# Performance work log

Measured on AMD Instinct MI355X. Metric: run time of the kernel, lower is better.

The kernel has to match this reference:

```python
import jax, jax.numpy as jnp
import numpy as np
from jax import lax

ALPHA = 1.5
N_ITER = 100


def entmax(z, alpha=ALPHA, n_iter=N_ITER):
    # z: [B, Sq, Sk] scores. Bisection for the entmax threshold tau.
    z = (alpha - 1.0) * z.astype(jnp.float32)
    S = z.shape[-1]
    z_max = jnp.max(z, axis=-1, keepdims=True)          # [B, Sq, 1]
    tau_min = z_max - 1.0
    tau_max = z_max - np.float32(S ** (1.0 - alpha))
    inv = 1.0 / (alpha - 1.0)                            # = 2.0 for alpha=1.5

    def body(carry, _):
        tmin, tmax, _ = carry
        tau = (tmin + tmax) * 0.5
        p = jnp.maximum(z - tau, 0.0) ** inv             # [B, Sq, Sk]
        Z = jnp.sum(p, axis=-1, keepdims=True)           # [B, Sq, 1]
        tmin = jnp.where(Z >= 1.0, tau, tmin)
        tmax = jnp.where(Z < 1.0, tau, tmax)
        return (tmin, tmax, tau), None

    init = (tau_min, tau_max, (tau_min + tau_max) * 0.5)
    (tmin, tmax, tau), _ = lax.scan(jax.checkpoint(body), init, None, length=n_iter)
    # faithful to the TF code: final output uses p, Z from the LAST iteration's tau
    p = jnp.maximum(z - tau, 0.0) ** inv
    Z = jnp.sum(p, axis=-1, keepdims=True)
    return p / Z


def setup_inputs() -> dict:
    key = jax.random.key(0)
    kq, kk, kv = jax.random.split(key, 3)
    B, S, D = 8, 2048, 128
    return {
        "query": jax.random.normal(kq, (B, S, D), dtype=jnp.float32),
        "key": jax.random.normal(kk, (B, S, D), dtype=jnp.float32),
        "value": jax.random.normal(kv, (B, S, D), dtype=jnp.float32),
    }


def reference(query, key, value):
    scores = jnp.einsum("bqd,bkd->bqk", query, key)      # QK^T, no scaling (as in source)
    weights = entmax(scores, alpha=ALPHA, n_iter=N_ITER)
    return jnp.einsum("bqk,bkd->bqd", weights, value)
```

## Files before the change

kernel.cpp:

```cpp
#include <hip/hip_runtime.h>

#define BB 8
#define SS 2048
#define DD 128
#define ROWS 16
#define NW 8
#define CTW 16

typedef short bf16x8 __attribute__((ext_vector_type(8)));
typedef float f32x4 __attribute__((ext_vector_type(4)));

template <int I> struct IC { static constexpr int value = I; };
template <int I, int N, typename F>
__device__ __forceinline__ void sfor(F&& f) {
  if constexpr (I < N) { f(IC<I>{}); sfor<I + 1, N>((F&&)f); }
}

__device__ __forceinline__ short f2bf(float x) {
  return __builtin_bit_cast(short, (__bf16)x);
}

__device__ __forceinline__ void stage_tile(const short* g, short* l) {
#pragma unroll
  for (int s = 0; s < 4; ++s) {
    __builtin_amdgcn_global_load_lds(
        (const __attribute__((address_space(1))) void*)(g + (s << 9)),
        (__attribute__((address_space(3))) void*)(l + (s << 9)), 16, 0, 0);
  }
}

__global__ __launch_bounds__(256)
void ksplit(const float* __restrict__ K, short* __restrict__ Khi) {
  const int lin = blockIdx.x * 256 + threadIdx.x;
  const int r   = lin >> 4;
  const int c8  = lin & 15;
  const float4 v0 = *(const float4*)(K + (size_t)lin * 8);
  const float4 v1 = *(const float4*)(K + (size_t)lin * 8 + 4);
  bf16x8 h;
  h[0] = f2bf(v0.x); h[1] = f2bf(v0.y); h[2] = f2bf(v0.z); h[3] = f2bf(v0.w);
  h[4] = f2bf(v1.x); h[5] = f2bf(v1.y); h[6] = f2bf(v1.z); h[7] = f2bf(v1.w);
  const int bct  = r >> 4;
  const int m16  = r & 15;
  const int s    = c8 >> 2;
  const int quad = c8 & 3;
  const size_t out = ((((size_t)bct * 4 + s) * 64) + quad * 16 + m16) * 8;
  *(bf16x8*)(Khi + out) = h;
}

__global__ __launch_bounds__(512) __attribute__((amdgpu_waves_per_eu(4)))
void attn(const float* __restrict__ Q, const short* __restrict__ Khi,
          const float* __restrict__ K, const float* __restrict__ V,
          float* __restrict__ Out) {
  __shared__ short kring[NW][2][2048];
  __shared__ unsigned short Qs[ROWS][136];
  __shared__ float rbuf[ROWS][64];
  __shared__ int   scol[ROWS][64];
  __shared__ float exM[NW][ROWS];
  __shared__ int   rcnt[ROWS];
  __shared__ int   rovf[ROWS];
  __shared__ float tauB[ROWS], ZB[ROWS];

  const int tid  = threadIdx.x;
  const int lane = tid & 63;
  const int wid  = __builtin_amdgcn_readfirstlane(tid >> 6);
  const int quad = lane >> 4, m16 = lane & 15;
  const int b    = blockIdx.x & 7;
  const int qt   = blockIdx.x >> 3;

  const float* Qb = Q + (size_t)(b * SS + qt * ROWS) * DD;
  const float* Kb = K + (size_t)b * SS * DD;
  const float* Vb = V + (size_t)b * SS * DD;
  float*       Ob = Out + (size_t)(b * SS + qt * ROWS) * DD;
  const short* KHb = Khi + (size_t)b * SS * DD;

  if (tid < ROWS) { rcnt[tid] = 0; rovf[tid] = 0; }

  {
    const int row = tid >> 5, d = (tid & 31) * 4;
    const float4 v = *(const float4*)&Qb[row * DD + d];
    ushort4 h;
    h.x = (unsigned short)f2bf(0.5f * v.x);
    h.y = (unsigned short)f2bf(0.5f * v.y);
    h.z = (unsigned short)f2bf(0.5f * v.z);
    h.w = (unsigned short)f2bf(0.5f * v.w);
    *(ushort4*)&Qs[row][d] = h;
  }
  __syncthreads();

  bf16x8 qh[4];
#pragma unroll
  for (int s = 0; s < 4; ++s)
    qh[s] = *(const bf16x8*)&Qs[m16][s * 32 + quad * 8];

  short* ring0 = &kring[wid][0][0];
  short* ring1 = &kring[wid][1][0];
  const short* gw = KHb + ((size_t)(wid * CTW) << 11) + lane * 8;

  stage_tile(gw + 0 * 2048, ring0);
  stage_tile(gw + 1 * 2048, ring1);

  f32x4 acc[CTW];
  sfor<0, CTW>([&](auto ic) {
    constexpr int i = ic.value;
    if constexpr (i < CTW - 1) asm volatile("s_waitcnt vmcnt(4)" ::: "memory");
    else                       asm volatile("s_waitcnt vmcnt(0)" ::: "memory");
    const short* sbl = ((i & 1) ? ring1 : ring0) + lane * 8;
    f32x4 c = {0.f, 0.f, 0.f, 0.f};
    sfor<0, 4>([&](auto sc) {
      constexpr int s = sc.value;
      const bf16x8 bh = *(const bf16x8*)(sbl + (s << 9));
      c = __builtin_amdgcn_mfma_f32_16x16x32_bf16(qh[s], bh, c, 0, 0, 0);
    });
    acc[i] = c;
    if constexpr (i + 2 < CTW) {
      asm volatile("s_waitcnt lgkmcnt(0)" ::: "memory");
      stage_tile(gw + (i + 2) * 2048, (i & 1) ? ring1 : ring0);
    }
  });

  float mx[4] = {-1e38f, -1e38f, -1e38f, -1e38f};
  sfor<0, CTW>([&](auto ic) {
#pragma unroll
    for (int j = 0; j < 4; ++j) mx[j] = fmaxf(mx[j], acc[ic.value][j]);
  });
#pragma unroll
  for (int j = 0; j < 4; ++j)
#pragma unroll
    for (int s = 1; s <= 8; s <<= 1) mx[j] = fmaxf(mx[j], __shfl_xor(mx[j], s));
  if (m16 == 0) {
#pragma unroll
    for (int j = 0; j < 4; ++j) exM[wid][4 * quad + j] = mx[j];
  }
  __syncthreads();
  float M4[4];
#pragma unroll
  for (int j = 0; j < 4; ++j) {
    float m = -1e38f;
#pragma unroll
    for (int w = 0; w < NW; ++w) m = fmaxf(m, exM[w][4 * quad + j]);
    M4[j] = m;
  }

  sfor<0, CTW>([&](auto ic) {
    constexpr int i = ic.value;
    const int col = wid * 256 + i * 16 + m16;
#pragma unroll
    for (int j = 0; j < 4; ++j) {
      const int row = 4 * quad + j;
      if (acc[i][j] > M4[j] - 1.25f) {
        const int pos = atomicAdd(&rcnt[row], 1);
        if (pos < 64) { scol[row][pos] = col; rbuf[row][pos] = acc[i][j]; }
        else rovf[row] = 1;
      }
    }
  });
  __syncthreads();

  const int rr32 = lane >> 5;
  const int row  = 2 * wid + rr32;
  const int l32  = lane & 31;
  const int nA = rcnt[2 * wid]     < 64 ? rcnt[2 * wid]     : 64;
  const int nB = rcnt[2 * wid + 1] < 64 ? rcnt[2 * wid + 1] : 64;
  const int nr  = rr32 ? nB : nA;
  const int nmx = nA > nB ? nA : nB;

  {
    const float4 q4 = *(const float4*)&Qb[row * DD + l32 * 4];
    for (int i = 0; i < nmx; ++i) {
      const bool act = i < nr;
      const int c = act ? scol[row][i] : scol[row][0];
      const float4 k4 = *(const float4*)&Kb[(size_t)c * DD + l32 * 4];
      float t = q4.x * k4.x + q4.y * k4.y + q4.z * k4.z + q4.w * k4.w;
#pragma unroll
      for (int s = 1; s <= 16; s <<= 1) t += __shfl_xor(t, s);
      if (act && l32 == 0) rbuf[row][i] = 0.5f * t;
    }
  }

  {
    const float z0 = (l32 < nr)      ? rbuf[row][l32]      : -1e38f;
    const float z1 = (l32 + 32 < nr) ? rbuf[row][l32 + 32] : -1e38f;
    float k0 = 0.f, S10 = 0.f, S20 = 0.f, nb0 = -1e38f;
    float k1 = 0.f, S11 = 0.f, S21 = 0.f, nb1 = -1e38f;
    for (int j = 0; j < nr; ++j) {
      const float w = rbuf[row][j];
      const bool ge0 = (w > z0) || (w == z0 && j <= l32);
      k0  += ge0 ? 1.f : 0.f;
      S10 += ge0 ? w : 0.f;
      S20  = ge0 ? fmaf(w, w, S20) : S20;
      nb0  = (!ge0 && w > nb0) ? w : nb0;
      const bool ge1 = (w > z1) || (w == z1 && j <= l32 + 32);
      k1  += ge1 ? 1.f : 0.f;
      S11 += ge1 ? w : 0.f;
      S21  = ge1 ? fmaf(w, w, S21) : S21;
      nb1  = (!ge1 && w > nb1) ? w : nb1;
    }
    const float d0 = fmaxf(fmaf(S10, S10, -k0 * (S20 - 1.f)), 0.f);
    const float d1 = fmaxf(fmaf(S11, S11, -k1 * (S21 - 1.f)), 0.f);
    const float tau0 = (S10 - __builtin_sqrtf(d0)) / fmaxf(k0, 1.f);
    const float tau1 = (S11 - __builtin_sqrtf(d1)) / fmaxf(k1, 1.f);
    const bool v0b = z0 > tau0, v1b = z1 > tau1;
    const bool v0  = v0b && (nb0 <= tau0);
    const bool v1  = v1b && (nb1 <= tau1);
    float tv = fmaxf(v0 ? tau0 : -1e38f, v1 ? tau1 : -1e38f);
    float tb = fmaxf(v0b ? tau0 : -1e38f, v1b ? tau1 : -1e38f);
#pragma unroll
    for (int s = 1; s <= 16; s <<= 1) {
      tv = fmaxf(tv, __shfl_xor(tv, s));
      tb = fmaxf(tb, __shfl_xor(tb, s));
    }
    const float tau = (tv > -1e37f) ? tv : tb;
    const float p0 = fmaxf(z0 - tau, 0.f);
    const float p1 = fmaxf(z1 - tau, 0.f);
    float zp = fmaf(p0, p0, p1 * p1);
#pragma unroll
    for (int s = 1; s <= 16; s <<= 1) zp += __shfl_xor(zp, s);
    if (l32 == 0) { tauB[row] = tau; ZB[row] = zp; }
  }

  if (!rovf[row]) {
    const float tau = tauB[row];
    const float iz  = 1.0f / ZB[row];
    float4 o = {0.f, 0.f, 0.f, 0.f};
    for (int i = 0; i < nr; ++i) {
      const float rv = rbuf[row][i];
      const float tt = fmaxf(rv - tau, 0.f);
      const float pi = tt * tt * iz;
      const int   c  = scol[row][i];
      const float4 v4 = *(const float4*)&Vb[(size_t)c * DD + l32 * 4];
      o.x = fmaf(pi, v4.x, o.x);
      o.y = fmaf(pi, v4.y, o.y);
      o.z = fmaf(pi, v4.z, o.z);
      o.w = fmaf(pi, v4.w, o.w);
    }
    *(float4*)&Ob[row * DD + l32 * 4] = o;
  }

#pragma unroll
  for (int rr = 0; rr < 2; ++rr) {
    const int frow = 2 * wid + rr;
    if (!rovf[frow]) continue;
    float* zr = (float*)&kring[wid][0][0];
    for (int c0 = 0; c0 < 32; ++c0) {
      const int c = c0 * 64 + lane;
      const float* kp = &Kb[(size_t)c * DD];
      float t = 0.f;
      for (int d = 0; d < DD; d += 4) {
        const float4 qv = *(const float4*)&Qb[frow * DD + d];
        const float4 kv = *(const float4*)&kp[d];
        t = fmaf(qv.x, kv.x, t); t = fmaf(qv.y, kv.y, t);
        t = fmaf(qv.z, kv.z, t); t = fmaf(qv.w, kv.w, t);
      }
      zr[c] = 0.5f * t;
    }
    float Mr = -1e38f;
    for (int c0 = 0; c0 < 32; ++c0) Mr = fmaxf(Mr, zr[c0 * 64 + lane]);
#pragma unroll
    for (int s = 1; s <= 32; s <<= 1) Mr = fmaxf(Mr, __shfl_xor(Mr, s));
    float tmn = Mr - 1.0f, tmx = Mr - 0.022097086912079608f;
    float tau = 0.5f * (tmn + tmx), Zr = 0.f;
    for (int it = 0; it < 100; ++it) {
      tau = 0.5f * (tmn + tmx);
      float zp = 0.f;
      for (int c0 = 0; c0 < 32; ++c0) {
        const float tt = fmaxf(zr[c0 * 64 + lane] - tau, 0.f);
        zp = fmaf(tt, tt, zp);
      }
#pragma unroll
      for (int s = 1; s <= 32; s <<= 1) zp += __shfl_xor(zp, s);
      Zr = zp;
      const float nmn = (zp >= 1.f) ? tau : tmn;
      const float nmx2 = (zp >= 1.f) ? tmx : tau;
      const bool ch = (nmn != tmn) || (nmx2 != tmx);
      tmn = nmn; tmx = nmx2;
      if (!__any(ch)) break;
    }
    const float iz = 1.0f / Zr;
    float2 o = {0.f, 0.f};
    for (int c = 0; c < SS; ++c) {
      const float tt = fmaxf(zr[c] - tau, 0.f);
      if (tt > 0.f) {
        const float pi = tt * tt * iz;
        const float2 v2 = *(const float2*)&Vb[(size_t)c * DD + lane * 2];
        o.x = fmaf(pi, v2.x, o.x);
        o.y = fmaf(pi, v2.y, o.y);
      }
    }
    *(float2*)&Ob[frow * DD + lane * 2] = o;
  }
}

extern "C" void kernel_launch(void* const* d_in, const int* in_sizes, int n_in,
                              void* d_out, int out_size, void* d_ws, size_t ws_size,
                              hipStream_t stream) {
  const float* Q = (const float*)d_in[0];
  const float* K = (const float*)d_in[1];
  const float* V = (const float*)d_in[2];
  float* out = (float*)d_out;
  short* Khi = (short*)d_ws;

  hipLaunchKernelGGL(ksplit, dim3(BB * SS * DD / (256 * 8)), dim3(256), 0, stream,
                     K, Khi);
  hipLaunchKernelGGL(attn, dim3(BB * (SS / ROWS)), dim3(512), 0, stream,
                     Q, Khi, K, V, out);
}
```

Measured before the change: 117.5 us.

## Halve warps per block and pack per-tile score accumulators as bf16 pairs

Each block now runs 4 waves of 256 threads instead of 8, and every wave scores 32 key tiles instead of 16. To keep register pressure down, the running row max is updated right after each MFMA and the tile scores are stored as packed bf16 pairs rather than fp32 vectors. Each wave then refines and finishes 4 query rows in two passes instead of 2. The candidate threshold is widened to M-1.35 to allow for bf16 rounding of the stored scores, which adds more candidates and a higher chance of falling back to the overflow path.

```diff
diff --git a/kernel.cpp b/kernel.cpp
--- a/kernel.cpp
+++ b/kernel.cpp
@@ -4,8 +4,8 @@
 #define SS 2048
 #define DD 128
 #define ROWS 16
-#define NW 8
-#define CTW 16
+#define NW 4
+#define CTW 32
 
 typedef short bf16x8 __attribute__((ext_vector_type(8)));
 typedef float f32x4 __attribute__((ext_vector_type(4)));
@@ -18,6 +18,10 @@
 
 __device__ __forceinline__ short f2bf(float x) {
   return __builtin_bit_cast(short, (__bf16)x);
+}
+__device__ __forceinline__ unsigned pk2(float a, float b) {
+  return (unsigned)(unsigned short)f2bf(a) |
+         ((unsigned)(unsigned short)f2bf(b) << 16);
 }
 
 __device__ __forceinline__ void stage_tile(const short* g, short* l) {
@@ -47,7 +51,7 @@
   *(bf16x8*)(Khi + out) = h;
 }
 
-__global__ __launch_bounds__(512) __attribute__((amdgpu_waves_per_eu(4)))
+__global__ __launch_bounds__(256) __attribute__((amdgpu_waves_per_eu(3, 4)))
 void attn(const float* __restrict__ Q, const short* __restrict__ Khi,
           const float* __restrict__ K, const float* __restrict__ V,
           float* __restrict__ Out) {
@@ -76,14 +80,20 @@
   if (tid < ROWS) { rcnt[tid] = 0; rovf[tid] = 0; }
 
   {
-    const int row = tid >> 5, d = (tid & 31) * 4;
-    const float4 v = *(const float4*)&Qb[row * DD + d];
-    ushort4 h;
-    h.x = (unsigned short)f2bf(0.5f * v.x);
-    h.y = (unsigned short)f2bf(0.5f * v.y);
-    h.z = (unsigned short)f2bf(0.5f * v.z);
-    h.w = (unsigned short)f2bf(0.5f * v.w);
-    *(ushort4*)&Qs[row][d] = h;
+    const int row = tid >> 4, d = (tid & 15) * 8;
+    const float4 v0 = *(const float4*)&Qb[row * DD + d];
+    const float4 v1 = *(const float4*)&Qb[row * DD + d + 4];
+    ushort4 h0, h1;
+    h0.x = (unsigned short)f2bf(0.5f * v0.x);
+    h0.y = (unsigned short)f2bf(0.5f * v0.y);
+    h0.z = (unsigned short)f2bf(0.5f * v0.z);
+    h0.w = (unsigned short)f2bf(0.5f * v0.w);
+    h1.x = (unsigned short)f2bf(0.5f * v1.x);
+    h1.y = (unsigned short)f2bf(0.5f * v1.y);
+    h1.z = (unsigned short)f2bf(0.5f * v1.z);
+    h1.w = (unsigned short)f2bf(0.5f * v1.w);
+    *(ushort4*)&Qs[row][d]     = h0;
+    *(ushort4*)&Qs[row][d + 4] = h1;
   }
   __syncthreads();
 
@@ -99,7 +109,9 @@
   stage_tile(gw + 0 * 2048, ring0);
   stage_tile(gw + 1 * 2048, ring1);
 
-  f32x4 acc[CTW];
+  unsigned zpk[CTW][2];
+  float mx[4] = {-1e38f, -1e38f, -1e38f, -1e38f};
+
   sfor<0, CTW>([&](auto ic) {
     constexpr int i = ic.value;
     if constexpr (i < CTW - 1) asm volatile("s_waitcnt vmcnt(4)" ::: "memory");
@@ -111,18 +123,16 @@
       const bf16x8 bh = *(const bf16x8*)(sbl + (s << 9));
       c = __builtin_amdgcn_mfma_f32_16x16x32_bf16(qh[s], bh, c, 0, 0, 0);
     });
-    acc[i] = c;
+#pragma unroll
+    for (int j = 0; j < 4; ++j) mx[j] = fmaxf(mx[j], c[j]);
+    zpk[i][0] = pk2(c[0], c[1]);
+    zpk[i][1] = pk2(c[2], c[3]);
     if constexpr (i + 2 < CTW) {
       asm volatile("s_waitcnt lgkmcnt(0)" ::: "memory");
       stage_tile(gw + (i + 2) * 2048, (i & 1) ? ring1 : ring0);
     }
   });
 
-  float mx[4] = {-1e38f, -1e38f, -1e38f, -1e38f};
-  sfor<0, CTW>([&](auto ic) {
-#pragma unroll
-    for (int j = 0; j < 4; ++j) mx[j] = fmaxf(mx[j], acc[ic.value][j]);
-  });
 #pragma unroll
   for (int j = 0; j < 4; ++j)
 #pragma unroll
@@ -141,15 +151,20 @@
     M4[j] = m;
   }
 
-  sfor<0, CTW>([&](auto ic) {
-    constexpr int i = ic.value;
-    const int col = wid * 256 + i * 16 + m16;
+  sfor<0, CTW>([&](auto cc) {
+    constexpr int ct = cc.value;
+    const int col = wid * 512 + ct * 16 + m16;
+    float v[4];
+    v[0] = __uint_as_float(zpk[ct][0] << 16);
+    v[1] = __uint_as_float(zpk[ct][0] & 0xffff0000u);
+    v[2] = __uint_as_float(zpk[ct][1] << 16);
+    v[3] = __uint_as_float(zpk[ct][1] & 0xffff0000u);
 #pragma unroll
     for (int j = 0; j < 4; ++j) {
       const int row = 4 * quad + j;
-      if (acc[i][j] > M4[j] - 1.25f) {
+      if (v[j] > M4[j] - 1.35f) {
         const int pos = atomicAdd(&rcnt[row], 1);
-        if (pos < 64) { scol[row][pos] = col; rbuf[row][pos] = acc[i][j]; }
+        if (pos < 64) { scol[row][pos] = col; rbuf[row][pos] = v[j]; }
         else rovf[row] = 1;
       }
     }
@@ -157,88 +172,92 @@
   __syncthreads();
 
   const int rr32 = lane >> 5;
-  const int row  = 2 * wid + rr32;
   const int l32  = lane & 31;
-  const int nA = rcnt[2 * wid]     < 64 ? rcnt[2 * wid]     : 64;
-  const int nB = rcnt[2 * wid + 1] < 64 ? rcnt[2 * wid + 1] : 64;
-  const int nr  = rr32 ? nB : nA;
-  const int nmx = nA > nB ? nA : nB;
-
-  {
-    const float4 q4 = *(const float4*)&Qb[row * DD + l32 * 4];
-    for (int i = 0; i < nmx; ++i) {
-      const bool act = i < nr;
-      const int c = act ? scol[row][i] : scol[row][0];
-      const float4 k4 = *(const float4*)&Kb[(size_t)c * DD + l32 * 4];
-      float t = q4.x * k4.x + q4.y * k4.y + q4.z * k4.z + q4.w * k4.w;
-#pragma unroll
-      for (int s = 1; s <= 16; s <<= 1) t += __shfl_xor(t, s);
-      if (act && l32 == 0) rbuf[row][i] = 0.5f * t;
-    }
-  }
-
-  {
-    const float z0 = (l32 < nr)      ? rbuf[row][l32]      : -1e38f;
-    const float z1 = (l32 + 32 < nr) ? rbuf[row][l32 + 32] : -1e38f;
-    float k0 = 0.f, S10 = 0.f, S20 = 0.f, nb0 = -1e38f;
-    float k1 = 0.f, S11 = 0.f, S21 = 0.f, nb1 = -1e38f;
-    for (int j = 0; j < nr; ++j) {
-      const float w = rbuf[row][j];
-      const bool ge0 = (w > z0) || (w == z0 && j <= l32);
-      k0  += ge0 ? 1.f : 0.f;
-      S10 += ge0 ? w : 0.f;
-      S20  = ge0 ? fmaf(w, w, S20) : S20;
-      nb0  = (!ge0 && w > nb0) ? w : nb0;
-      const bool ge1 = (w > z1) || (w == z1 && j <= l32 + 32);
-      k1  += ge1 ? 1.f : 0.f;
-      S11 += ge1 ? w : 0.f;
-      S21  = ge1 ? fmaf(w, w, S21) : S21;
-      nb1  = (!ge1 && w > nb1) ? w : nb1;
-    }
-    const float d0 = fmaxf(fmaf(S10, S10, -k0 * (S20 - 1.f)), 0.f);
-    const float d1 = fmaxf(fmaf(S11, S11, -k1 * (S21 - 1.f)), 0.f);
-    const float tau0 = (S10 - __builtin_sqrtf(d0)) / fmaxf(k0, 1.f);
-    const float tau1 = (S11 - __builtin_sqrtf(d1)) / fmaxf(k1, 1.f);
-    const bool v0b = z0 > tau0, v1b = z1 > tau1;
-    const bool v0  = v0b && (nb0 <= tau0);
-    const bool v1  = v1b && (nb1 <= tau1);
-    float tv = fmaxf(v0 ? tau0 : -1e38f, v1 ? tau1 : -1e38f);
-    float tb = fmaxf(v0b ? tau0 : -1e38f, v1b ? tau1 : -1e38f);
-#pragma unroll
-    for (int s = 1; s <= 16; s <<= 1) {
-      tv = fmaxf(tv, __shfl_xor(tv, s));
-      tb = fmaxf(tb, __shfl_xor(tb, s));
-    }
-    const float tau = (tv > -1e37f) ? tv : tb;
-    const float p0 = fmaxf(z0 - tau, 0.f);
-    const float p1 = fmaxf(z1 - tau, 0.f);
-    float zp = fmaf(p0, p0, p1 * p1);
-#pragma unroll
-    for (int s = 1; s <= 16; s <<= 1) zp += __shfl_xor(zp, s);
-    if (l32 == 0) { tauB[row] = tau; ZB[row] = zp; }
-  }
-
-  if (!rovf[row]) {
-    const float tau = tauB[row];
-    const float iz  = 1.0f / ZB[row];
-    float4 o = {0.f, 0.f, 0.f, 0.f};
-    for (int i = 0; i < nr; ++i) {
-      const float rv = rbuf[row][i];
-      const float tt = fmaxf(rv - tau, 0.f);
-      const float pi = tt * tt * iz;
-      const int   c  = scol[row][i];
-      const float4 v4 = *(const float4*)&Vb[(size_t)c * DD + l32 * 4];
-      o.x = fmaf(pi, v4.x, o.x);
-      o.y = fmaf(pi, v4.y, o.y);
-      o.z = fmaf(pi, v4.z, o.z);
-      o.w = fmaf(pi, v4.w, o.w);
-    }
-    *(float4*)&Ob[row * DD + l32 * 4] = o;
-  }
-
-#pragma unroll
-  for (int rr = 0; rr < 2; ++rr) {
-    const int frow = 2 * wid + rr;
+
+#pragma unroll
+  for (int p = 0; p < 2; ++p) {
+    const int row = 4 * wid + 2 * p + rr32;
+    const int nA = rcnt[4 * wid + 2 * p]     < 64 ? rcnt[4 * wid + 2 * p]     : 64;
+    const int nB = rcnt[4 * wid + 2 * p + 1] < 64 ? rcnt[4 * wid + 2 * p + 1] : 64;
+    const int nr  = rr32 ? nB : nA;
+    const int nmx = nA > nB ? nA : nB;
+
+    {
+      const float4 q4 = *(const float4*)&Qb[row * DD + l32 * 4];
+      for (int i = 0; i < nmx; ++i) {
+        const bool act = i < nr;
+        const int c = act ? scol[row][i] : scol[row][0];
+        const float4 k4 = *(const float4*)&Kb[(size_t)c * DD + l32 * 4];
+        float t = q4.x * k4.x + q4.y * k4.y + q4.z * k4.z + q4.w * k4.w;
+#pragma unroll
+        for (int s = 1; s <= 16; s <<= 1) t += __shfl_xor(t, s);
+        if (act && l32 == 0) rbuf[row][i] = 0.5f * t;
+      }
+    }
+
+    {
+      const float z0 = (l32 < nr)      ? rbuf[row][l32]      : -1e38f;
+      const float z1 = (l32 + 32 < nr) ? rbuf[row][l32 + 32] : -1e38f;
+      float k0 = 0.f, S10 = 0.f, S20 = 0.f, nb0 = -1e38f;
+      float k1 = 0.f, S11 = 0.f, S21 = 0.f, nb1 = -1e38f;
+      for (int j = 0; j < nr; ++j) {
+        const float w = rbuf[row][j];
+        const bool ge0 = (w > z0) || (w == z0 && j <= l32);
+        k0  += ge0 ? 1.f : 0.f;
+        S10 += ge0 ? w : 0.f;
+        S20  = ge0 ? fmaf(w, w, S20) : S20;
+        nb0  = (!ge0 && w > nb0) ? w : nb0;
+        const bool ge1 = (w > z1) || (w == z1 && j <= l32 + 32);
+        k1  += ge1 ? 1.f : 0.f;
+        S11 += ge1 ? w : 0.f;
+        S21  = ge1 ? fmaf(w, w, S21) : S21;
+        nb1  = (!ge1 && w > nb1) ? w : nb1;
+      }
+      const float d0 = fmaxf(fmaf(S10, S10, -k0 * (S20 - 1.f)), 0.f);
+      const float d1 = fmaxf(fmaf(S11, S11, -k1 * (S21 - 1.f)), 0.f);
+      const float tau0 = (S10 - __builtin_sqrtf(d0)) / fmaxf(k0, 1.f);
+      const float tau1 = (S11 - __builtin_sqrtf(d1)) / fmaxf(k1, 1.f);
+      const bool v0b = z0 > tau0, v1b = z1 > tau1;
+      const bool v0  = v0b && (nb0 <= tau0);
+      const bool v1  = v1b && (nb1 <= tau1);
+      float tv = fmaxf(v0 ? tau0 : -1e38f, v1 ? tau1 : -1e38f);
+      float tb = fmaxf(v0b ? tau0 : -1e38f, v1b ? tau1 : -1e38f);
+#pragma unroll
+      for (int s = 1; s <= 16; s <<= 1) {
+        tv = fmaxf(tv, __shfl_xor(tv, s));
+        tb = fmaxf(tb, __shfl_xor(tb, s));
+      }
+      const float tau = (tv > -1e37f) ? tv : tb;
+      const float p0 = fmaxf(z0 - tau, 0.f);
+      const float p1 = fmaxf(z1 - tau, 0.f);
+      float zp = fmaf(p0, p0, p1 * p1);
+#pragma unroll
+      for (int s = 1; s <= 16; s <<= 1) zp += __shfl_xor(zp, s);
+      if (l32 == 0) { tauB[row] = tau; ZB[row] = zp; }
+    }
+
+    if (!rovf[row]) {
+      const float tau = tauB[row];
+      const float iz  = 1.0f / ZB[row];
+      float4 o = {0.f, 0.f, 0.f, 0.f};
+      for (int i = 0; i < nr; ++i) {
+        const float rv = rbuf[row][i];
+        const float tt = fmaxf(rv - tau, 0.f);
+        const float pi = tt * tt * iz;
+        const int   c  = scol[row][i];
+        const float4 v4 = *(const float4*)&Vb[(size_t)c * DD + l32 * 4];
+        o.x = fmaf(pi, v4.x, o.x);
+        o.y = fmaf(pi, v4.y, o.y);
+        o.z = fmaf(pi, v4.z, o.z);
+        o.w = fmaf(pi, v4.w, o.w);
+      }
+      *(float4*)&Ob[row * DD + l32 * 4] = o;
+    }
+  }
+
+#pragma unroll
+  for (int rr = 0; rr < 4; ++rr) {
+    const int frow = 4 * wid + rr;
     if (!rovf[frow]) continue;
     float* zr = (float*)&kring[wid][0][0];
     for (int c0 = 0; c0 < 32; ++c0) {
@@ -301,6 +320,6 @@
 
   hipLaunchKernelGGL(ksplit, dim3(BB * SS * DD / (256 * 8)), dim3(256), 0, stream,
                      K, Khi);
-  hipLaunchKernelGGL(attn, dim3(BB * (SS / ROWS)), dim3(512), 0, stream,
+  hipLaunchKernelGGL(attn, dim3(BB * (SS / ROWS)), dim3(256), 0, stream,
                      Q, Khi, K, V, out);
 }
```

After: 127.6 us. 8.6% more time.
